# Performance work log

Hardware: AMD Instinct MI355X
Metric: run time of the kernel (lower is better)

The kernel has to match this reference:

```python
import jax, jax.numpy as jnp
import numpy as np

N_NODES = 50000
N_EDGES = 800000
IN_FEATS = 256
OUT_FEATS = 64


def setup_inputs() -> dict:
    key = jax.random.key(0)
    k1, k2, k3, k4, k5 = jax.random.split(key, 5)
    h = jax.random.normal(k1, (N_NODES, IN_FEATS), dtype=jnp.float32)
    norm = jax.random.uniform(k2, (N_NODES,), dtype=jnp.float32)
    src = jax.random.randint(k3, (N_EDGES,), 0, N_NODES, dtype=jnp.int32)
    dst = jax.random.randint(k4, (N_EDGES,), 0, N_NODES, dtype=jnp.int32)
    # xavier_uniform for weight [in, out]
    limit = float(np.sqrt(6.0 / (IN_FEATS + OUT_FEATS)))
    weight = jax.random.uniform(k5, (IN_FEATS, OUT_FEATS), dtype=jnp.float32,
                                minval=-limit, maxval=limit)
    bias = jnp.zeros((OUT_FEATS,), dtype=jnp.float32)
    return {"h": h, "norm": norm, "src": src, "dst": dst,
            "weight": weight, "bias": bias}


def reference(h, norm, src, dst, weight, bias):
    # h: [N, in], weight: [in, out] -> projected node features [N, out]
    hw = jnp.matmul(h, weight)
    # message per edge: h_src * norm_src  -> [E, out]
    msg = hw[src] * norm[src][:, None]
    # sum over in-neighbors of each dst node -> [N, out]
    agg = jax.ops.segment_sum(msg, dst, num_segments=N_NODES)
    # scale by dst norm, add bias, activation
    out = agg * norm[:, None] + bias
    return jax.nn.relu(out)
```

## Files before the change

kernel.cpp:

```cpp
#include <hip/hip_runtime.h>

#define K_FEATS 256
#define C_FEATS 64
#define RCHUNK 1024
#define RROUNDS (RCHUNK / 64)
#define NDIGIT 1024
#define LCAP 2048

typedef __attribute__((ext_vector_type(8))) short short8;
typedef __attribute__((ext_vector_type(8))) unsigned short ushort8;
typedef __attribute__((ext_vector_type(4))) float f32x4;

__device__ __forceinline__ unsigned short f2bf(float f) {
    union { float f; unsigned u; } v; v.f = f;
    unsigned r = v.u + 0x7FFF + ((v.u >> 16) & 1);
    return (unsigned short)(r >> 16);
}


__global__ __launch_bounds__(256) void packhist_kernel(
    const int* __restrict__ dst, unsigned* __restrict__ chunkhist_cm, int n_edges)
{
    __shared__ unsigned cnt[NDIGIT];
    const int tid = threadIdx.x;
    #pragma unroll
    for (int j = 0; j < NDIGIT / 256; ++j) cnt[tid + j * 256] = 0;
    __syncthreads();
    const int e0 = blockIdx.x * RCHUNK + tid * 4;
    if (e0 + 3 < n_edges) {
        const int4 d4 = *reinterpret_cast<const int4*>(dst + e0);
        atomicAdd(&cnt[d4.x >> 6], 1);
        atomicAdd(&cnt[d4.y >> 6], 1);
        atomicAdd(&cnt[d4.z >> 6], 1);
        atomicAdd(&cnt[d4.w >> 6], 1);
    } else {
        #pragma unroll
        for (int j = 0; j < 4; ++j) {
            if (e0 + j < n_edges) atomicAdd(&cnt[dst[e0 + j] >> 6], 1);
        }
    }
    __syncthreads();
    uint4 o;
    o.x = cnt[tid * 4 + 0]; o.y = cnt[tid * 4 + 1];
    o.z = cnt[tid * 4 + 2]; o.w = cnt[tid * 4 + 3];
    *reinterpret_cast<uint4*>(&chunkhist_cm[(size_t)blockIdx.x * NDIGIT + tid * 4]) = o;
}

__global__ __launch_bounds__(256) void transpose_hist_kernel(
    const unsigned* __restrict__ in_cm, unsigned* __restrict__ out_dm, int nchunk)
{
    __shared__ unsigned t[64][65];
    const int tid = threadIdx.x;
    const int tx = tid & 63, ty = tid >> 6;
    const int dig0 = blockIdx.x * 64;
    const int c0   = blockIdx.y * 64;
    #pragma unroll
    for (int j = 0; j < 16; ++j) {
        const int c = c0 + ty + j * 4;
        if (c < nchunk) t[ty + j * 4][tx] = in_cm[(size_t)c * NDIGIT + dig0 + tx];
    }
    __syncthreads();
    const int c = c0 + tx;
    if (c < nchunk) {
        #pragma unroll
        for (int j = 0; j < 16; ++j) {
            const int dig = dig0 + ty + j * 4;
            out_dm[(size_t)dig * nchunk + c] = t[tx][ty + j * 4];
        }
    }
}

__global__ __launch_bounds__(256) void scan_block_kernel(
    const int* in, int* out, int* bsum, int n)
{
    __shared__ int s[256];
    const int tid = threadIdx.x;
    const int i = blockIdx.x * 256 + tid;
    const int v = (i < n) ? in[i] : 0;
    s[tid] = v;
    __syncthreads();
    #pragma unroll
    for (int d = 1; d < 256; d <<= 1) {
        int t = (tid >= d) ? s[tid - d] : 0;
        __syncthreads();
        s[tid] += t;
        __syncthreads();
    }
    if (i < n) out[i] = s[tid] - v;
    if (tid == 255) bsum[blockIdx.x] = s[255];
}

__global__ __launch_bounds__(256) void scan_partials_kernel(int* __restrict__ bsum, int nb)
{
    __shared__ int s[256];
    const int tid = threadIdx.x;
    int v[16];
    int sum = 0;
    #pragma unroll
    for (int j = 0; j < 16; ++j) {
        const int i = tid * 16 + j;
        v[j] = (i < nb) ? bsum[i] : 0;
        sum += v[j];
    }
    s[tid] = sum;
    __syncthreads();
    #pragma unroll
    for (int d = 1; d < 256; d <<= 1) {
        int t = (tid >= d) ? s[tid - d] : 0;
        __syncthreads();
        s[tid] += t;
        __syncthreads();
    }
    int base = s[tid] - sum;
    #pragma unroll
    for (int j = 0; j < 16; ++j) {
        const int i = tid * 16 + j;
        if (i < nb) { bsum[i] = base; base += v[j]; }
    }
}

__global__ __launch_bounds__(256) void transpose_w_digbase_kernel(
    const float* __restrict__ w, unsigned short* __restrict__ wt,
    const unsigned* __restrict__ choff, const int* __restrict__ bsum2,
    int* __restrict__ digbase, int n_edges, int nchunk)
{
    const int gid = blockIdx.x * 256 + threadIdx.x;
    if (gid < NDIGIT) {
        const int gi = gid * nchunk;
        digbase[gid] = (int)choff[gi] + bsum2[gi >> 8];
    }
    if (gid == 0) digbase[NDIGIT] = n_edges;

    const int e2 = gid * 4;
    #pragma unroll
    for (int j = 0; j < 4; ++j) {
        const int idx = e2 + j;
        const int col = idx >> 8, k = idx & 255;
        wt[idx] = f2bf(w[k * C_FEATS + col]);
    }
}

__global__ __launch_bounds__(256) void gemm_mfma_kernel(
    const float* __restrict__ h, const unsigned short* __restrict__ wt_g,
    const float* __restrict__ norm, unsigned short* __restrict__ hwn, int n_nodes)
{
    __shared__ __align__(16) unsigned char lds[65536];

    const int tid  = threadIdx.x;
    const int row0 = blockIdx.x * 64;

    #pragma unroll
    for (int j = 0; j < 8; ++j) {
        const int ch = j * 256 + tid;
        const int r = ch >> 5, k0 = (ch & 31) * 8;
        const int row = row0 + r;
        ushort8 v;
        if (row < n_nodes) {
            const float4 f0 = *reinterpret_cast<const float4*>(h + (size_t)row * K_FEATS + k0);
            const float4 f1 = *reinterpret_cast<const float4*>(h + (size_t)row * K_FEATS + k0 + 4);
            v[0]=f2bf(f0.x); v[1]=f2bf(f0.y); v[2]=f2bf(f0.z); v[3]=f2bf(f0.w);
            v[4]=f2bf(f1.x); v[5]=f2bf(f1.y); v[6]=f2bf(f1.z); v[7]=f2bf(f1.w);
        } else {
            v = (ushort8)0;
        }
        const int addr = (r * 512 + k0 * 2) ^ ((r & 7) << 4);
        *reinterpret_cast<ushort8*>(lds + addr) = v;
    }
    #pragma unroll
    for (int j = 0; j < 8; ++j) {
        const int ch = j * 256 + tid;
        const int col = ch >> 5, k0 = (ch & 31) * 8;
        const ushort8 v = *reinterpret_cast<const ushort8*>(wt_g + ch * 8);
        const int addr = 32768 + ((col * 512 + k0 * 2) ^ ((col & 7) << 4));
        *reinterpret_cast<ushort8*>(lds + addr) = v;
    }
    __syncthreads();

    const int lane = tid & 63, w = tid >> 6;
    const int r16 = lane & 15, kg = lane >> 4;
    const int x = (r16 & 7) << 4;

    f32x4 acc[4];
    #pragma unroll
    for (int n = 0; n < 4; ++n) acc[n] = (f32x4)0.f;

    #pragma unroll
    for (int kb = 0; kb < 8; ++kb) {
        const int common = (r16 * 512 + kb * 64 + kg * 16) ^ x;
        const short8 a = *reinterpret_cast<const short8*>(lds + w * 8192 + common);
        #pragma unroll
        for (int n = 0; n < 4; ++n) {
            const short8 b = *reinterpret_cast<const short8*>(lds + 32768 + n * 8192 + common);
            acc[n] = __builtin_amdgcn_mfma_f32_16x16x32_bf16(a, b, acc[n], 0, 0, 0);
        }
    }

    #pragma unroll
    for (int i = 0; i < 4; ++i) {
        const int row = row0 + w * 16 + kg * 4 + i;
        if (row < n_nodes) {
            const float nv = norm[row];
            #pragma unroll
            for (int n = 0; n < 4; ++n) {
                hwn[(size_t)row * C_FEATS + n * 16 + r16] = f2bf(acc[n][i] * nv);
            }
        }
    }
}

__global__ __launch_bounds__(64) void rreorder_pass(
    const int* __restrict__ src, const int* __restrict__ dst,
    unsigned* __restrict__ P1, const unsigned* __restrict__ choff,
    const int* __restrict__ bsum2, int n_edges, int nchunk)
{
    __shared__ unsigned cnt[NDIGIT];
    const int c = blockIdx.x;
    const int lane = threadIdx.x;
    #pragma unroll
    for (int j = 0; j < NDIGIT / 64; ++j) cnt[lane + j * 64] = 0;
    __syncthreads();
    const int base = c * RCHUNK;

    unsigned dA = 0, sA = 0, dB = 0, sB = 0;
    if (base + lane < n_edges)      { dA = dst[base + lane];      sA = src[base + lane]; }
    if (base + 64 + lane < n_edges) { dB = dst[base + 64 + lane]; sB = src[base + 64 + lane]; }

    for (int r = 0; r < RROUNDS; ++r) {
        unsigned dC = 0, sC = 0;
        const int idxC = base + (r + 2) * 64 + lane;
        if (r + 2 < RROUNDS && idxC < n_edges) { dC = dst[idxC]; sC = src[idxC]; }

        const int idx = base + r * 64 + lane;
        const bool valid = idx < n_edges;
        const int g = valid ? (int)(dA >> 6) : NDIGIT;
        unsigned long long m = ~0ull;
        #pragma unroll
        for (int b = 0; b < 11; ++b) {
            const unsigned long long bb = __ballot((g >> b) & 1);
            m &= ((g >> b) & 1) ? bb : ~bb;
        }
        const unsigned long long below = m & ((1ull << lane) - 1ull);
        const int laneRank = __popcll(below);
        const int total = __popcll(m);
        const bool isFirst = (below == 0ull);
        unsigned oldc = 0;
        if (valid) oldc = cnt[g];
        __syncthreads();
        if (valid) {
            const int gi = g * nchunk + c;
            const unsigned slot = choff[gi] + (unsigned)bsum2[gi >> 8]
                                + oldc + (unsigned)laneRank;
            P1[slot] = ((dA & 63u) << 16) | sA;
            if (isFirst) cnt[g] = oldc + (unsigned)total;
        }
        __syncthreads();
        dA = dB; sA = sB; dB = dC; sB = sC;
    }
}

__global__ __launch_bounds__(512) void aggregate_kernel(
    const uint2* __restrict__ hwn2, const unsigned* __restrict__ P1,
    const int* __restrict__ digbase,
    const float* __restrict__ norm, const float* __restrict__ bias,
    float* __restrict__ out, int n_nodes)
{
    __shared__ unsigned stage[LCAP];
    __shared__ unsigned short lsrc[LCAP];
    __shared__ int cnt64[64];
    __shared__ int cur64[64];
    __shared__ int segbase[65];

    const int tid = threadIdx.x;
    const int b = blockIdx.x;
    const int n0 = b * 64;

    const int s = digbase[b];
    const int bucketsz = digbase[b + 1] - s;

    if (tid < 64) { cnt64[tid] = 0; cur64[tid] = 0; }
    __syncthreads();

    const int lane = tid & 63;
    const int wv = tid >> 6;
    const int q  = lane >> 4;
    const int c4 = lane & 15;

    if (bucketsz <= LCAP) {
        for (int i = tid; i < bucketsz; i += 512) {
            const unsigned key = P1[s + i];
            stage[i] = key;
            atomicAdd(&cnt64[key >> 16], 1);
        }
        __syncthreads();
        if (tid < 64) {
            int x = cnt64[tid];
            #pragma unroll
            for (int d = 1; d < 64; d <<= 1) {
                const int t = __shfl_up(x, d);
                if (tid >= d) x += t;
            }
            segbase[tid + 1] = x;
            if (tid == 0) segbase[0] = 0;
        }
        __syncthreads();
        for (int i = tid; i < bucketsz; i += 512) {
            const unsigned key = stage[i];
            const int nn = key >> 16;
            const int pos = atomicAdd(&cur64[nn], 1);
            lsrc[segbase[nn] + pos] = (unsigned short)key;
        }
        __syncthreads();
        for (int nn = wv; nn < 64; nn += 8) {
            const int node = n0 + nn;
            if (node >= n_nodes) break;
            const int ls = segbase[nn];
            const int le = segbase[nn + 1];
            float a0 = 0.f, a1 = 0.f, a2 = 0.f, a3 = 0.f;
            int e = ls + q;
            for (; e + 4 < le; e += 8) {
                const uint2 u = hwn2[(size_t)lsrc[e] * 16 + c4];
                const uint2 v = hwn2[(size_t)lsrc[e + 4] * 16 + c4];
                a0 += __uint_as_float(u.x << 16) + __uint_as_float(v.x << 16);
                a1 += __uint_as_float(u.x & 0xFFFF0000u) + __uint_as_float(v.x & 0xFFFF0000u);
                a2 += __uint_as_float(u.y << 16) + __uint_as_float(v.y << 16);
                a3 += __uint_as_float(u.y & 0xFFFF0000u) + __uint_as_float(v.y & 0xFFFF0000u);
            }
            for (; e < le; e += 4) {
                const uint2 u = hwn2[(size_t)lsrc[e] * 16 + c4];
                a0 += __uint_as_float(u.x << 16);
                a1 += __uint_as_float(u.x & 0xFFFF0000u);
                a2 += __uint_as_float(u.y << 16);
                a3 += __uint_as_float(u.y & 0xFFFF0000u);
            }
            a0 += __shfl_xor(a0, 16); a1 += __shfl_xor(a1, 16);
            a2 += __shfl_xor(a2, 16); a3 += __shfl_xor(a3, 16);
            a0 += __shfl_xor(a0, 32); a1 += __shfl_xor(a1, 32);
            a2 += __shfl_xor(a2, 32); a3 += __shfl_xor(a3, 32);
            if (q == 0) {
                const float nv = norm[node];
                const float4 bv = *reinterpret_cast<const float4*>(bias + c4 * 4);
                float4 o;
                o.x = fmaxf(fmaf(a0, nv, bv.x), 0.f);
                o.y = fmaxf(fmaf(a1, nv, bv.y), 0.f);
                o.z = fmaxf(fmaf(a2, nv, bv.z), 0.f);
                o.w = fmaxf(fmaf(a3, nv, bv.w), 0.f);
                *reinterpret_cast<float4*>(out + (size_t)node * C_FEATS + c4 * 4) = o;
            }
        }
    } else {
        for (int nn = wv; nn < 64; nn += 8) {
            const int node = n0 + nn;
            if (node >= n_nodes) break;
            float a0 = 0.f, a1 = 0.f, a2 = 0.f, a3 = 0.f;
            for (int i = q; i < bucketsz; i += 4) {
                const unsigned key = P1[s + i];
                if ((int)(key >> 16) == nn) {
                    const uint2 u = hwn2[(size_t)(key & 0xFFFFu) * 16 + c4];
                    a0 += __uint_as_float(u.x << 16);
                    a1 += __uint_as_float(u.x & 0xFFFF0000u);
                    a2 += __uint_as_float(u.y << 16);
                    a3 += __uint_as_float(u.y & 0xFFFF0000u);
                }
            }
            a0 += __shfl_xor(a0, 16); a1 += __shfl_xor(a1, 16);
            a2 += __shfl_xor(a2, 16); a3 += __shfl_xor(a3, 16);
            a0 += __shfl_xor(a0, 32); a1 += __shfl_xor(a1, 32);
            a2 += __shfl_xor(a2, 32); a3 += __shfl_xor(a3, 32);
            if (q == 0) {
                const float nv = norm[node];
                const float4 bv = *reinterpret_cast<const float4*>(bias + c4 * 4);
                float4 o;
                o.x = fmaxf(fmaf(a0, nv, bv.x), 0.f);
                o.y = fmaxf(fmaf(a1, nv, bv.y), 0.f);
                o.z = fmaxf(fmaf(a2, nv, bv.z), 0.f);
                o.w = fmaxf(fmaf(a3, nv, bv.w), 0.f);
                *reinterpret_cast<float4*>(out + (size_t)node * C_FEATS + c4 * 4) = o;
            }
        }
    }
}

extern "C" void kernel_launch(void* const* d_in, const int* in_sizes, int n_in,
                              void* d_out, int out_size, void* d_ws, size_t ws_size,
                              hipStream_t stream) {
    const float* h      = (const float*)d_in[0];
    const float* norm   = (const float*)d_in[1];
    const int*   src    = (const int*)d_in[2];
    const int*   dst    = (const int*)d_in[3];
    const float* weight = (const float*)d_in[4];
    const float* bias   = (const float*)d_in[5];

    const int n_nodes = in_sizes[1];
    const int n_edges = in_sizes[2];

    char* ws = (char*)d_ws;
    unsigned* P1            = (unsigned*)(ws + 0);
    unsigned* chunkhist_cm  = (unsigned*)(ws + 3200000);
    unsigned* chunkhist_dm  = (unsigned*)(ws + 6403072);
    unsigned short* hwn     = (unsigned short*)(ws + 3200000);
    int* bsum2              = (int*)(ws + 9606144);
    int* digbase            = (int*)(ws + 9618656);
    unsigned short* wt_g    = (unsigned short*)(ws + 9622784);

    const int nchunk  = (n_edges + RCHUNK - 1) / RCHUNK;
    const int nscan   = NDIGIT * nchunk;
    const int nb_r    = (nscan + 255) / 256;
    const int ngroup  = (n_nodes + 63) / 64;

    packhist_kernel<<<nchunk, 256, 0, stream>>>(dst, chunkhist_cm, n_edges);

    {
        dim3 g(NDIGIT / 64, (nchunk + 63) / 64);
        transpose_hist_kernel<<<g, 256, 0, stream>>>(chunkhist_cm, chunkhist_dm, nchunk);
    }

    scan_block_kernel<<<nb_r, 256, 0, stream>>>((int*)chunkhist_dm, (int*)chunkhist_dm, bsum2, nscan);
    scan_partials_kernel<<<1, 256, 0, stream>>>(bsum2, nb_r);

    transpose_w_digbase_kernel<<<16, 256, 0, stream>>>(
        weight, wt_g, chunkhist_dm, bsum2, digbase, n_edges, nchunk);

    rreorder_pass<<<nchunk, 64, 0, stream>>>(src, dst, P1, chunkhist_dm, bsum2, n_edges, nchunk);

    gemm_mfma_kernel<<<(n_nodes + 63) / 64, 256, 0, stream>>>(h, wt_g, norm, hwn, n_nodes);

    aggregate_kernel<<<ngroup, 512, 0, stream>>>(
        (const uint2*)hwn, P1, digbase, norm, bias, (float*)d_out, n_nodes);
}
```

Baseline: 85.00 us.

## Halve radix digits, fuse histogram transpose into scan, widen aggregate gathers

Changes the destination bucketing from 64-node to 128-node groups, which halves the number of digits and the size of the chunk histogram. The separate transpose kernel is removed and the scan kernel now reads the chunk-major histogram with a strided transposed index, saving one launch and one pass over the histogram. The aggregate kernel handles 128 nodes per block and gathers 16-byte rows with 8 lanes per edge instead of 8-byte rows with 16 lanes. In exchange, the scan's strided reads are uncoalesced, and the larger buckets risk exceeding LCAP more often, which sends those blocks down the slow fallback path.

Measured after the change: 84.17 us. Within noise of the previous version (-1.0%).

```diff
diff --git a/kernel.cpp b/kernel.cpp
--- a/kernel.cpp
+++ b/kernel.cpp
@@ -4,8 +4,10 @@
 #define C_FEATS 64
 #define RCHUNK 1024
 #define RROUNDS (RCHUNK / 64)
-#define NDIGIT 1024
-#define LCAP 2048
+#define NDIGIT 512
+#define DSHIFT 7
+#define NMASK 127
+#define LCAP 2560
 
 typedef __attribute__((ext_vector_type(8))) short short8;
 typedef __attribute__((ext_vector_type(8))) unsigned short ushort8;
@@ -17,6 +19,9 @@
     return (unsigned short)(r >> 16);
 }
 
+__device__ __forceinline__ float bflo(unsigned u) { return __uint_as_float(u << 16); }
+__device__ __forceinline__ float bfhi(unsigned u) { return __uint_as_float(u & 0xFFFF0000u); }
+
 
 __global__ __launch_bounds__(256) void packhist_kernel(
     const int* __restrict__ dst, unsigned* __restrict__ chunkhist_cm, int n_edges)
@@ -29,54 +34,35 @@
     const int e0 = blockIdx.x * RCHUNK + tid * 4;
     if (e0 + 3 < n_edges) {
         const int4 d4 = *reinterpret_cast<const int4*>(dst + e0);
-        atomicAdd(&cnt[d4.x >> 6], 1);
-        atomicAdd(&cnt[d4.y >> 6], 1);
-        atomicAdd(&cnt[d4.z >> 6], 1);
-        atomicAdd(&cnt[d4.w >> 6], 1);
+        atomicAdd(&cnt[d4.x >> DSHIFT], 1);
+        atomicAdd(&cnt[d4.y >> DSHIFT], 1);
+        atomicAdd(&cnt[d4.z >> DSHIFT], 1);
+        atomicAdd(&cnt[d4.w >> DSHIFT], 1);
     } else {
         #pragma unroll
         for (int j = 0; j < 4; ++j) {
-            if (e0 + j < n_edges) atomicAdd(&cnt[dst[e0 + j] >> 6], 1);
-        }
-    }
-    __syncthreads();
-    uint4 o;
-    o.x = cnt[tid * 4 + 0]; o.y = cnt[tid * 4 + 1];
-    o.z = cnt[tid * 4 + 2]; o.w = cnt[tid * 4 + 3];
-    *reinterpret_cast<uint4*>(&chunkhist_cm[(size_t)blockIdx.x * NDIGIT + tid * 4]) = o;
-}
-
-__global__ __launch_bounds__(256) void transpose_hist_kernel(
-    const unsigned* __restrict__ in_cm, unsigned* __restrict__ out_dm, int nchunk)
-{
-    __shared__ unsigned t[64][65];
-    const int tid = threadIdx.x;
-    const int tx = tid & 63, ty = tid >> 6;
-    const int dig0 = blockIdx.x * 64;
-    const int c0   = blockIdx.y * 64;
-    #pragma unroll
-    for (int j = 0; j < 16; ++j) {
-        const int c = c0 + ty + j * 4;
-        if (c < nchunk) t[ty + j * 4][tx] = in_cm[(size_t)c * NDIGIT + dig0 + tx];
-    }
-    __syncthreads();
-    const int c = c0 + tx;
-    if (c < nchunk) {
-        #pragma unroll
-        for (int j = 0; j < 16; ++j) {
-            const int dig = dig0 + ty + j * 4;
-            out_dm[(size_t)dig * nchunk + c] = t[tx][ty + j * 4];
-        }
-    }
-}
-
-__global__ __launch_bounds__(256) void scan_block_kernel(
-    const int* in, int* out, int* bsum, int n)
+            if (e0 + j < n_edges) atomicAdd(&cnt[dst[e0 + j] >> DSHIFT], 1);
+        }
+    }
+    __syncthreads();
+    uint2 o;
+    o.x = cnt[tid * 2 + 0]; o.y = cnt[tid * 2 + 1];
+    *reinterpret_cast<uint2*>(&chunkhist_cm[(size_t)blockIdx.x * NDIGIT + tid * 2]) = o;
+}
+
+__global__ __launch_bounds__(256) void scan_block_t_kernel(
+    const unsigned* __restrict__ in_cm, int* __restrict__ out_dm,
+    int* __restrict__ bsum, int n, int nchunk)
 {
     __shared__ int s[256];
     const int tid = threadIdx.x;
     const int i = blockIdx.x * 256 + tid;
-    const int v = (i < n) ? in[i] : 0;
+    int v = 0;
+    if (i < n) {
+        const int dig = i / nchunk;
+        const int c   = i - dig * nchunk;
+        v = (int)in_cm[(size_t)c * NDIGIT + dig];
+    }
     s[tid] = v;
     __syncthreads();
     #pragma unroll
@@ -86,7 +72,7 @@
         s[tid] += t;
         __syncthreads();
     }
-    if (i < n) out[i] = s[tid] - v;
+    if (i < n) out_dm[i] = s[tid] - v;
     if (tid == 255) bsum[blockIdx.x] = s[255];
 }
 
@@ -232,10 +218,10 @@
 
         const int idx = base + r * 64 + lane;
         const bool valid = idx < n_edges;
-        const int g = valid ? (int)(dA >> 6) : NDIGIT;
+        const int g = valid ? (int)(dA >> DSHIFT) : NDIGIT;
         unsigned long long m = ~0ull;
         #pragma unroll
-        for (int b = 0; b < 11; ++b) {
+        for (int b = 0; b < 10; ++b) {
             const unsigned long long bb = __ballot((g >> b) & 1);
             m &= ((g >> b) & 1) ? bb : ~bb;
         }
@@ -250,7 +236,7 @@
             const int gi = g * nchunk + c;
             const unsigned slot = choff[gi] + (unsigned)bsum2[gi >> 8]
                                 + oldc + (unsigned)laneRank;
-            P1[slot] = ((dA & 63u) << 16) | sA;
+            P1[slot] = ((dA & (unsigned)NMASK) << 16) | sA;
             if (isFirst) cnt[g] = oldc + (unsigned)total;
         }
         __syncthreads();
@@ -259,122 +245,144 @@
 }
 
 __global__ __launch_bounds__(512) void aggregate_kernel(
-    const uint2* __restrict__ hwn2, const unsigned* __restrict__ P1,
+    const uint4* __restrict__ hwn4, const unsigned* __restrict__ P1,
     const int* __restrict__ digbase,
     const float* __restrict__ norm, const float* __restrict__ bias,
     float* __restrict__ out, int n_nodes)
 {
     __shared__ unsigned stage[LCAP];
     __shared__ unsigned short lsrc[LCAP];
-    __shared__ int cnt64[64];
-    __shared__ int cur64[64];
-    __shared__ int segbase[65];
+    __shared__ int cnt128[128];
+    __shared__ int cur128[128];
+    __shared__ int segbase[129];
 
     const int tid = threadIdx.x;
     const int b = blockIdx.x;
-    const int n0 = b * 64;
+    const int n0 = b * 128;
 
     const int s = digbase[b];
     const int bucketsz = digbase[b + 1] - s;
 
-    if (tid < 64) { cnt64[tid] = 0; cur64[tid] = 0; }
+    if (tid < 128) { cnt128[tid] = 0; cur128[tid] = 0; }
     __syncthreads();
 
     const int lane = tid & 63;
     const int wv = tid >> 6;
-    const int q  = lane >> 4;
-    const int c4 = lane & 15;
+    const int q  = lane >> 3;
+    const int c8 = lane & 7;
 
     if (bucketsz <= LCAP) {
         for (int i = tid; i < bucketsz; i += 512) {
             const unsigned key = P1[s + i];
             stage[i] = key;
-            atomicAdd(&cnt64[key >> 16], 1);
+            atomicAdd(&cnt128[key >> 16], 1);
         }
         __syncthreads();
         if (tid < 64) {
-            int x = cnt64[tid];
+            const int a = cnt128[2 * tid], bb = cnt128[2 * tid + 1];
+            int p = a + bb;
             #pragma unroll
             for (int d = 1; d < 64; d <<= 1) {
-                const int t = __shfl_up(x, d);
-                if (tid >= d) x += t;
-            }
-            segbase[tid + 1] = x;
-            if (tid == 0) segbase[0] = 0;
+                const int t = __shfl_up(p, d);
+                if (tid >= d) p += t;
+            }
+            segbase[2 * tid]     = p - a - bb;
+            segbase[2 * tid + 1] = p - bb;
+            if (tid == 63) segbase[128] = p;
         }
         __syncthreads();
         for (int i = tid; i < bucketsz; i += 512) {
             const unsigned key = stage[i];
             const int nn = key >> 16;
-            const int pos = atomicAdd(&cur64[nn], 1);
+            const int pos = atomicAdd(&cur128[nn], 1);
             lsrc[segbase[nn] + pos] = (unsigned short)key;
         }
         __syncthreads();
-        for (int nn = wv; nn < 64; nn += 8) {
+        for (int nn = wv; nn < 128; nn += 8) {
             const int node = n0 + nn;
             if (node >= n_nodes) break;
             const int ls = segbase[nn];
             const int le = segbase[nn + 1];
-            float a0 = 0.f, a1 = 0.f, a2 = 0.f, a3 = 0.f;
+            float a0=0.f,a1=0.f,a2=0.f,a3=0.f,a4=0.f,a5=0.f,a6=0.f,a7=0.f;
             int e = ls + q;
-            for (; e + 4 < le; e += 8) {
-                const uint2 u = hwn2[(size_t)lsrc[e] * 16 + c4];
-                const uint2 v = hwn2[(size_t)lsrc[e + 4] * 16 + c4];
-                a0 += __uint_as_float(u.x << 16) + __uint_as_float(v.x << 16);
-                a1 += __uint_as_float(u.x & 0xFFFF0000u) + __uint_as_float(v.x & 0xFFFF0000u);
-                a2 += __uint_as_float(u.y << 16) + __uint_as_float(v.y << 16);
-                a3 += __uint_as_float(u.y & 0xFFFF0000u) + __uint_as_float(v.y & 0xFFFF0000u);
-            }
-            for (; e < le; e += 4) {
-                const uint2 u = hwn2[(size_t)lsrc[e] * 16 + c4];
-                a0 += __uint_as_float(u.x << 16);
-                a1 += __uint_as_float(u.x & 0xFFFF0000u);
-                a2 += __uint_as_float(u.y << 16);
-                a3 += __uint_as_float(u.y & 0xFFFF0000u);
-            }
-            a0 += __shfl_xor(a0, 16); a1 += __shfl_xor(a1, 16);
-            a2 += __shfl_xor(a2, 16); a3 += __shfl_xor(a3, 16);
-            a0 += __shfl_xor(a0, 32); a1 += __shfl_xor(a1, 32);
-            a2 += __shfl_xor(a2, 32); a3 += __shfl_xor(a3, 32);
+            for (; e + 8 < le; e += 16) {
+                const uint4 u = hwn4[(size_t)lsrc[e] * 8 + c8];
+                const uint4 v = hwn4[(size_t)lsrc[e + 8] * 8 + c8];
+                a0 += bflo(u.x) + bflo(v.x); a1 += bfhi(u.x) + bfhi(v.x);
+                a2 += bflo(u.y) + bflo(v.y); a3 += bfhi(u.y) + bfhi(v.y);
+                a4 += bflo(u.z) + bflo(v.z); a5 += bfhi(u.z) + bfhi(v.z);
+                a6 += bflo(u.w) + bflo(v.w); a7 += bfhi(u.w) + bfhi(v.w);
+            }
+            for (; e < le; e += 8) {
+                const uint4 u = hwn4[(size_t)lsrc[e] * 8 + c8];
+                a0 += bflo(u.x); a1 += bfhi(u.x);
+                a2 += bflo(u.y); a3 += bfhi(u.y);
+                a4 += bflo(u.z); a5 += bfhi(u.z);
+                a6 += bflo(u.w); a7 += bfhi(u.w);
+            }
+            #pragma unroll
+            for (int d = 8; d < 64; d <<= 1) {
+                a0 += __shfl_xor(a0, d); a1 += __shfl_xor(a1, d);
+                a2 += __shfl_xor(a2, d); a3 += __shfl_xor(a3, d);
+                a4 += __shfl_xor(a4, d); a5 += __shfl_xor(a5, d);
+                a6 += __shfl_xor(a6, d); a7 += __shfl_xor(a7, d);
+            }
             if (q == 0) {
                 const float nv = norm[node];
-                const float4 bv = *reinterpret_cast<const float4*>(bias + c4 * 4);
-                float4 o;
-                o.x = fmaxf(fmaf(a0, nv, bv.x), 0.f);
-                o.y = fmaxf(fmaf(a1, nv, bv.y), 0.f);
-                o.z = fmaxf(fmaf(a2, nv, bv.z), 0.f);
-                o.w = fmaxf(fmaf(a3, nv, bv.w), 0.f);
-                *reinterpret_cast<float4*>(out + (size_t)node * C_FEATS + c4 * 4) = o;
+                const float4 b0 = *reinterpret_cast<const float4*>(bias + c8 * 8);
+                const float4 b1 = *reinterpret_cast<const float4*>(bias + c8 * 8 + 4);
+                float4 o0, o1;
+                o0.x = fmaxf(fmaf(a0, nv, b0.x), 0.f);
+                o0.y = fmaxf(fmaf(a1, nv, b0.y), 0.f);
+                o0.z = fmaxf(fmaf(a2, nv, b0.z), 0.f);
+                o0.w = fmaxf(fmaf(a3, nv, b0.w), 0.f);
+                o1.x = fmaxf(fmaf(a4, nv, b1.x), 0.f);
+                o1.y = fmaxf(fmaf(a5, nv, b1.y), 0.f);
+                o1.z = fmaxf(fmaf(a6, nv, b1.z), 0.f);
+                o1.w = fmaxf(fmaf(a7, nv, b1.w), 0.f);
+                float* po = out + (size_t)node * C_FEATS + c8 * 8;
+                *reinterpret_cast<float4*>(po)     = o0;
+                *reinterpret_cast<float4*>(po + 4) = o1;
             }
         }
     } else {
-        for (int nn = wv; nn < 64; nn += 8) {
+        for (int nn = wv; nn < 128; nn += 8) {
             const int node = n0 + nn;
             if (node >= n_nodes) break;
-            float a0 = 0.f, a1 = 0.f, a2 = 0.f, a3 = 0.f;
-            for (int i = q; i < bucketsz; i += 4) {
+            float a0=0.f,a1=0.f,a2=0.f,a3=0.f,a4=0.f,a5=0.f,a6=0.f,a7=0.f;
+            for (int i = q; i < bucketsz; i += 8) {
                 const unsigned key = P1[s + i];
                 if ((int)(key >> 16) == nn) {
-                    const uint2 u = hwn2[(size_t)(key & 0xFFFFu) * 16 + c4];
-                    a0 += __uint_as_float(u.x << 16);
-                    a1 += __uint_as_float(u.x & 0xFFFF0000u);
-                    a2 += __uint_as_float(u.y << 16);
-                    a3 += __uint_as_float(u.y & 0xFFFF0000u);
+                    const uint4 u = hwn4[(size_t)(key & 0xFFFFu) * 8 + c8];
+                    a0 += bflo(u.x); a1 += bfhi(u.x);
+                    a2 += bflo(u.y); a3 += bfhi(u.y);
+                    a4 += bflo(u.z); a5 += bfhi(u.z);
+                    a6 += bflo(u.w); a7 += bfhi(u.w);
                 }
             }
-            a0 += __shfl_xor(a0, 16); a1 += __shfl_xor(a1, 16);
-            a2 += __shfl_xor(a2, 16); a3 += __shfl_xor(a3, 16);
-            a0 += __shfl_xor(a0, 32); a1 += __shfl_xor(a1, 32);
-            a2 += __shfl_xor(a2, 32); a3 += __shfl_xor(a3, 32);
+            #pragma unroll
+            for (int d = 8; d < 64; d <<= 1) {
+                a0 += __shfl_xor(a0, d); a1 += __shfl_xor(a1, d);
+                a2 += __shfl_xor(a2, d); a3 += __shfl_xor(a3, d);
+                a4 += __shfl_xor(a4, d); a5 += __shfl_xor(a5, d);
+                a6 += __shfl_xor(a6, d); a7 += __shfl_xor(a7, d);
+            }
             if (q == 0) {
                 const float nv = norm[node];
-                const float4 bv = *reinterpret_cast<const float4*>(bias + c4 * 4);
-                float4 o;
-                o.x = fmaxf(fmaf(a0, nv, bv.x), 0.f);
-                o.y = fmaxf(fmaf(a1, nv, bv.y), 0.f);
-                o.z = fmaxf(fmaf(a2, nv, bv.z), 0.f);
-                o.w = fmaxf(fmaf(a3, nv, bv.w), 0.f);
-                *reinterpret_cast<float4*>(out + (size_t)node * C_FEATS + c4 * 4) = o;
+                const float4 b0 = *reinterpret_cast<const float4*>(bias + c8 * 8);
+                const float4 b1 = *reinterpret_cast<const float4*>(bias + c8 * 8 + 4);
+                float4 o0, o1;
+                o0.x = fmaxf(fmaf(a0, nv, b0.x), 0.f);
+                o0.y = fmaxf(fmaf(a1, nv, b0.y), 0.f);
+                o0.z = fmaxf(fmaf(a2, nv, b0.z), 0.f);
+                o0.w = fmaxf(fmaf(a3, nv, b0.w), 0.f);
+                o1.x = fmaxf(fmaf(a4, nv, b1.x), 0.f);
+                o1.y = fmaxf(fmaf(a5, nv, b1.y), 0.f);
+                o1.z = fmaxf(fmaf(a6, nv, b1.z), 0.f);
+                o1.w = fmaxf(fmaf(a7, nv, b1.w), 0.f);
+                float* po = out + (size_t)node * C_FEATS + c8 * 8;
+                *reinterpret_cast<float4*>(po)     = o0;
+                *reinterpret_cast<float4*>(po + 4) = o1;
             }
         }
     }
@@ -396,7 +404,7 @@
     char* ws = (char*)d_ws;
     unsigned* P1            = (unsigned*)(ws + 0);
     unsigned* chunkhist_cm  = (unsigned*)(ws + 3200000);
-    unsigned* chunkhist_dm  = (unsigned*)(ws + 6403072);
+    unsigned* chunkhist_dm  = (unsigned*)(ws + 4801536);
     unsigned short* hwn     = (unsigned short*)(ws + 3200000);
     int* bsum2              = (int*)(ws + 9606144);
     int* digbase            = (int*)(ws + 9618656);
@@ -405,16 +413,12 @@
     const int nchunk  = (n_edges + RCHUNK - 1) / RCHUNK;
     const int nscan   = NDIGIT * nchunk;
     const int nb_r    = (nscan + 255) / 256;
-    const int ngroup  = (n_nodes + 63) / 64;
+    const int ngroup  = (n_nodes + 127) / 128;
 
     packhist_kernel<<<nchunk, 256, 0, stream>>>(dst, chunkhist_cm, n_edges);
 
-    {
-        dim3 g(NDIGIT / 64, (nchunk + 63) / 64);
-        transpose_hist_kernel<<<g, 256, 0, stream>>>(chunkhist_cm, chunkhist_dm, nchunk);
-    }
-
-    scan_block_kernel<<<nb_r, 256, 0, stream>>>((int*)chunkhist_dm, (int*)chunkhist_dm, bsum2, nscan);
+    scan_block_t_kernel<<<nb_r, 256, 0, stream>>>(chunkhist_cm, (int*)chunkhist_dm,
+                                                  bsum2, nscan, nchunk);
     scan_partials_kernel<<<1, 256, 0, stream>>>(bsum2, nb_r);
 
     transpose_w_digbase_kernel<<<16, 256, 0, stream>>>(
@@ -425,5 +429,5 @@
     gemm_mfma_kernel<<<(n_nodes + 63) / 64, 256, 0, stream>>>(h, wt_g, norm, hwn, n_nodes);
 
     aggregate_kernel<<<ngroup, 512, 0, stream>>>(
-        (const uint2*)hwn, P1, digbase, norm, bias, (float*)d_out, n_nodes);
-}
+        (const uint4*)hwn, P1, digbase, norm, bias, (float*)d_out, n_nodes);
+}
```
